# Optimization experiments

Measured on AMD Instinct MI355X. Metric: run time of the kernel, lower is better.

The kernel has to match this reference:

```python
import jax, jax.numpy as jnp
import numpy as np

N = 50000
E = 800000
D_IN, D_HID, D_OUT = 256, 512, 256
LN_EPS = 1e-5


def setup_inputs() -> dict:
    key = jax.random.key(0)
    ks = jax.random.split(key, 8)
    return {
        "v": jax.random.normal(ks[0], (N, D_IN), dtype=jnp.float32),
        "edge_weight": jax.random.uniform(ks[1], (E,), dtype=jnp.float32),
        "epsilon": jnp.zeros((1, 1), dtype=jnp.float32),
        "w1": jax.random.normal(ks[2], (D_HID, D_IN), dtype=jnp.float32) * (1.0 / np.sqrt(D_IN)),
        "b1": jnp.zeros((D_HID,), dtype=jnp.float32),
        "g1": jnp.ones((D_HID,), dtype=jnp.float32),
        "beta1": jnp.zeros((D_HID,), dtype=jnp.float32),
        "w2": jax.random.normal(ks[3], (D_OUT, D_HID), dtype=jnp.float32) * (1.0 / np.sqrt(D_HID)),
        "b2": jnp.zeros((D_OUT,), dtype=jnp.float32),
        "g2": jnp.ones((D_OUT,), dtype=jnp.float32),
        "beta2": jnp.zeros((D_OUT,), dtype=jnp.float32),
        "src": jax.random.randint(ks[4], (E,), 0, N, dtype=jnp.int32),
        "dst": jax.random.randint(ks[5], (E,), 0, N, dtype=jnp.int32),
    }


def _layer_norm(x, g, b):
    mu = jnp.mean(x, axis=-1, keepdims=True)
    var = jnp.mean(jnp.square(x - mu), axis=-1, keepdims=True)
    return (x - mu) * jax.lax.rsqrt(var + LN_EPS) * g + b


def reference(v, edge_weight, epsilon, w1, b1, g1, beta1, w2, b2, g2, beta2, src, dst):
    # sparse adjacency aggregation: agg[dst] += w * v[src]   (torch.sparse.mm(a, v))
    msgs = v[src] * edge_weight[:, None]            # [E, D_IN]
    agg = jax.ops.segment_sum(msgs, dst, num_segments=v.shape[0])  # [N, D_IN]
    h = agg + epsilon * v                            # epsilon residual
    # MLP: Linear -> LayerNorm -> ReLU  (x2)
    h = jax.nn.relu(_layer_norm(h @ w1.T + b1, g1, beta1))
    h = jax.nn.relu(_layer_norm(h @ w2.T + b2, g2, beta2))
    return h
```

## Files before the change

### kernel.cpp

```cpp
#include <hip/hip_runtime.h>

#define D_IN 256
#define D_HID 512
#define D_OUT 256
#define LN_EPS 1e-5f
#define SCAN_B 512

typedef __attribute__((ext_vector_type(8))) short bf16x8;
typedef __attribute__((ext_vector_type(4))) float f32x4;

__device__ __forceinline__ ushort f2bf(float x) {
    union { float f; unsigned u; } c; c.f = x;
    unsigned r = c.u + 0x7FFFu + ((c.u >> 16) & 1u);
    return (ushort)(r >> 16);
}
__device__ __forceinline__ float bf2f(unsigned b) {
    union { unsigned u; float f; } c; c.u = b << 16;
    return c.f;
}

__global__ void zero_kernel(int* __restrict__ p, int n) {
    int i = blockIdx.x * 256 + threadIdx.x;
    if (i < n) p[i] = 0;
}

__global__ void hist_kernel(const int* __restrict__ dst, int* __restrict__ cnt, int E) {
    int e = blockIdx.x * 256 + threadIdx.x;
    if (e < E) atomicAdd(&cnt[dst[e]], 1);
}

__global__ __launch_bounds__(SCAN_B) void scan1_kernel(const int* __restrict__ cnt,
                                                       int* __restrict__ offs,
                                                       int* __restrict__ bsum, int n) {
    __shared__ int s[SCAN_B];
    int i = blockIdx.x * SCAN_B + threadIdx.x;
    int x = (i < n) ? cnt[i] : 0;
    s[threadIdx.x] = x;
    __syncthreads();
    for (int o = 1; o < SCAN_B; o <<= 1) {
        int t = (threadIdx.x >= (unsigned)o) ? s[threadIdx.x - o] : 0;
        __syncthreads();
        s[threadIdx.x] += t;
        __syncthreads();
    }
    if (i < n) offs[i] = s[threadIdx.x] - x;
    if (threadIdx.x == SCAN_B - 1) bsum[blockIdx.x] = s[threadIdx.x];
}

__global__ __launch_bounds__(128) void scan2_kernel(int* __restrict__ bsum, int nb) {
    __shared__ int s[128];
    int x = (threadIdx.x < (unsigned)nb) ? bsum[threadIdx.x] : 0;
    s[threadIdx.x] = x;
    __syncthreads();
    for (int o = 1; o < 128; o <<= 1) {
        int t = (threadIdx.x >= (unsigned)o) ? s[threadIdx.x - o] : 0;
        __syncthreads();
        s[threadIdx.x] += t;
        __syncthreads();
    }
    if (threadIdx.x < (unsigned)nb) bsum[threadIdx.x] = s[threadIdx.x] - x;
}

__global__ __launch_bounds__(SCAN_B) void scan3_kernel(int* __restrict__ offs,
                                                       int* __restrict__ cursor,
                                                       const int* __restrict__ bsum,
                                                       int n, int E) {
    int i = blockIdx.x * SCAN_B + threadIdx.x;
    if (i < n) {
        int v0 = offs[i] + bsum[blockIdx.x];
        offs[i] = v0;
        cursor[i] = v0;
    }
    if (i == 0) offs[n] = E;
}

__global__ void fill_kernel(const int* __restrict__ src, const int* __restrict__ dst,
                            const float* __restrict__ ew, int* __restrict__ cursor,
                            int2* __restrict__ perm, int E) {
    int e = blockIdx.x * 256 + threadIdx.x;
    if (e >= E) return;
    int p = atomicAdd(&cursor[dst[e]], 1);
    perm[p] = make_int2(src[e], __float_as_int(ew[e]));
}

__global__ void cvt_bf16_kernel(const float* __restrict__ in, ushort* __restrict__ out, int n4) {
    int i = blockIdx.x * 256 + threadIdx.x;
    if (i >= n4) return;
    float4 x = ((const float4*)in)[i];
    ((ushort4*)out)[i] = make_ushort4(f2bf(x.x), f2bf(x.y), f2bf(x.z), f2bf(x.w));
}

__global__ void cvt_w_kernel(const float* __restrict__ w1, const float* __restrict__ w2,
                             ushort* __restrict__ w1b, ushort* __restrict__ w2b) {
    int i = blockIdx.x * 256 + threadIdx.x;
    const float* src; ushort* dst; int j;
    if (i < 32768) { src = w1; dst = w1b; j = i; }
    else           { src = w2; dst = w2b; j = i - 32768; }
    float4 x = ((const float4*)src)[j];
    ((ushort4*)dst)[j] = make_ushort4(f2bf(x.x), f2bf(x.y), f2bf(x.z), f2bf(x.w));
}

__global__ __launch_bounds__(256) void aggregate_kernel(
    const ushort* __restrict__ vb, const float* __restrict__ eps_p,
    const int* __restrict__ offs, const int2* __restrict__ perm,
    ushort* __restrict__ aggb, int N) {
    int node = blockIdx.x * 4 + (threadIdx.x >> 6);
    if (node >= N) return;
    int lane = threadIdx.x & 63;
    int beg = offs[node], end = offs[node + 1];
    float a0 = 0.f, a1 = 0.f, a2 = 0.f, a3 = 0.f;

    int i = beg;
    for (; i + 4 <= end; i += 4) {
        int2 p0 = perm[i + 0], p1 = perm[i + 1], p2 = perm[i + 2], p3 = perm[i + 3];
        float w0 = __int_as_float(p0.y), w1 = __int_as_float(p1.y);
        float w2 = __int_as_float(p2.y), w3 = __int_as_float(p3.y);
        ushort4 r0 = ((const ushort4*)(vb + (size_t)p0.x * D_IN))[lane];
        ushort4 r1 = ((const ushort4*)(vb + (size_t)p1.x * D_IN))[lane];
        ushort4 r2 = ((const ushort4*)(vb + (size_t)p2.x * D_IN))[lane];
        ushort4 r3 = ((const ushort4*)(vb + (size_t)p3.x * D_IN))[lane];
        a0 += w0 * bf2f(r0.x) + w1 * bf2f(r1.x) + w2 * bf2f(r2.x) + w3 * bf2f(r3.x);
        a1 += w0 * bf2f(r0.y) + w1 * bf2f(r1.y) + w2 * bf2f(r2.y) + w3 * bf2f(r3.y);
        a2 += w0 * bf2f(r0.z) + w1 * bf2f(r1.z) + w2 * bf2f(r2.z) + w3 * bf2f(r3.z);
        a3 += w0 * bf2f(r0.w) + w1 * bf2f(r1.w) + w2 * bf2f(r2.w) + w3 * bf2f(r3.w);
    }
    for (; i < end; ++i) {
        int2 p = perm[i];
        float w = __int_as_float(p.y);
        ushort4 r = ((const ushort4*)(vb + (size_t)p.x * D_IN))[lane];
        a0 += w * bf2f(r.x); a1 += w * bf2f(r.y);
        a2 += w * bf2f(r.z); a3 += w * bf2f(r.w);
    }
    float eps = eps_p[0];
    ushort4 m = ((const ushort4*)(vb + (size_t)node * D_IN))[lane];
    a0 += eps * bf2f(m.x); a1 += eps * bf2f(m.y);
    a2 += eps * bf2f(m.z); a3 += eps * bf2f(m.w);
    ((ushort4*)(aggb + (size_t)node * D_IN))[lane] =
        make_ushort4(f2bf(a0), f2bf(a1), f2bf(a2), f2bf(a3));
}

template <int COLS, int WRITE_BF16>
__global__ __launch_bounds__(256) void gemm_ln_kernel(
    const ushort* __restrict__ A, const ushort* __restrict__ B,
    const float* __restrict__ bias, const float* __restrict__ g,
    const float* __restrict__ beta, void* __restrict__ Cv, int M, int K) {
    constexpr int CW = COLS / 4;
    constexpr int CF = CW / 16;
    __shared__ ushort As[32 * 32];
    __shared__ ushort Bs[COLS * 32];
    __shared__ float red[2][32][4];
    __shared__ float mu_s[32], rs_s[32];

    int t = threadIdx.x;
    int w = t >> 6, lane = t & 63;
    int row0 = blockIdx.x * 32;
    int fr = lane & 15, q = lane >> 4, kb = q * 8;
    int lrow = lane >> 2;
    int lcol = (lane & 3) * 8;

    f32x4 acc[2][CF];
    #pragma unroll
    for (int i = 0; i < 2; ++i)
        #pragma unroll
        for (int c = 0; c < CF; ++c) {
            f32x4 z = {0.f, 0.f, 0.f, 0.f};
            acc[i][c] = z;
        }

    for (int k0 = 0; k0 < K; k0 += 32) {
        #pragma unroll
        for (int c = 0; c < CF; ++c) {
            int br = w * CW + c * 16 + lrow;
            const ushort* gp = B + (size_t)br * K + k0 + lcol;
            __builtin_amdgcn_global_load_lds(
                (const __attribute__((address_space(1))) void*)gp,
                (__attribute__((address_space(3))) void*)(&Bs[(w * CW + c * 16) * 32]),
                16, 0, 0);
        }
        if (w < 2) {
            int ar = row0 + w * 16 + lrow;
            if (ar > M - 1) ar = M - 1;
            const ushort* gp = A + (size_t)ar * K + k0 + lcol;
            __builtin_amdgcn_global_load_lds(
                (const __attribute__((address_space(1))) void*)gp,
                (__attribute__((address_space(3))) void*)(&As[(w * 16) * 32]),
                16, 0, 0);
        }
        __syncthreads();

        bf16x8 af[2], bf[CF];
        af[0] = *(const bf16x8*)&As[fr * 32 + kb];
        af[1] = *(const bf16x8*)&As[(16 + fr) * 32 + kb];
        #pragma unroll
        for (int c = 0; c < CF; ++c)
            bf[c] = *(const bf16x8*)&Bs[(w * CW + c * 16 + fr) * 32 + kb];
        #pragma unroll
        for (int i = 0; i < 2; ++i)
            #pragma unroll
            for (int c = 0; c < CF; ++c)
                acc[i][c] = __builtin_amdgcn_mfma_f32_16x16x32_bf16(af[i], bf[c], acc[i][c], 0, 0, 0);
        __syncthreads();
    }

    float bi[CF], gg[CF], bb[CF];
    #pragma unroll
    for (int c = 0; c < CF; ++c) {
        int col = w * CW + c * 16 + fr;
        bi[c] = bias[col]; gg[c] = g[col]; bb[c] = beta[col];
    }

    #pragma unroll
    for (int i = 0; i < 2; ++i) {
        #pragma unroll
        for (int r = 0; r < 4; ++r) {
            float s = 0.f, sq = 0.f;
            #pragma unroll
            for (int c = 0; c < CF; ++c) {
                float x = acc[i][c][r] + bi[c];
                acc[i][c][r] = x;
                s += x; sq += x * x;
            }
            #pragma unroll
            for (int o = 1; o < 16; o <<= 1) {
                s  += __shfl_xor(s, o, 64);
                sq += __shfl_xor(sq, o, 64);
            }
            if (fr == 0) {
                int row = i * 16 + q * 4 + r;
                red[0][row][w] = s;
                red[1][row][w] = sq;
            }
        }
    }
    __syncthreads();
    if (t < 32) {
        float s  = red[0][t][0] + red[0][t][1] + red[0][t][2] + red[0][t][3];
        float sq = red[1][t][0] + red[1][t][1] + red[1][t][2] + red[1][t][3];
        float mu = s / (float)COLS;
        float var = sq / (float)COLS - mu * mu;
        mu_s[t] = mu;
        rs_s[t] = rsqrtf(var + LN_EPS);
    }
    __syncthreads();

    #pragma unroll
    for (int i = 0; i < 2; ++i) {
        #pragma unroll
        for (int r = 0; r < 4; ++r) {
            int row = i * 16 + q * 4 + r;
            int grow = row0 + row;
            if (grow >= M) continue;
            float mu = mu_s[row], rs = rs_s[row];
            #pragma unroll
            for (int c = 0; c < CF; ++c) {
                int col = w * CW + c * 16 + fr;
                float y = (acc[i][c][r] - mu) * rs * gg[c] + bb[c];
                y = fmaxf(y, 0.f);
                if (WRITE_BF16)
                    ((ushort*)Cv)[(size_t)grow * COLS + col] = f2bf(y);
                else
                    ((float*)Cv)[(size_t)grow * COLS + col] = y;
            }
        }
    }
}

extern "C" void kernel_launch(void* const* d_in, const int* in_sizes, int n_in,
                              void* d_out, int out_size, void* d_ws, size_t ws_size,
                              hipStream_t stream) {
    const float* v     = (const float*)d_in[0];
    const float* ew    = (const float*)d_in[1];
    const float* eps   = (const float*)d_in[2];
    const float* w1    = (const float*)d_in[3];
    const float* b1    = (const float*)d_in[4];
    const float* g1    = (const float*)d_in[5];
    const float* beta1 = (const float*)d_in[6];
    const float* w2    = (const float*)d_in[7];
    const float* b2    = (const float*)d_in[8];
    const float* g2    = (const float*)d_in[9];
    const float* beta2 = (const float*)d_in[10];
    const int*   src   = (const int*)d_in[11];
    const int*   dst   = (const int*)d_in[12];

    int N = in_sizes[0] / D_IN;
    int E = in_sizes[1];

    float* out = (float*)d_out;

    char* ws = (char*)d_ws;
    size_t off = 0;
    ushort* vb   = (ushort*)(ws + off); off += (size_t)N * D_IN * 2;
    ushort* aggb = (ushort*)(ws + off); off += (size_t)N * D_IN * 2;
    ushort* h1b  = (ushort*)(ws + off); off += (size_t)N * D_HID * 2;
    ushort* w1b  = (ushort*)(ws + off); off += (size_t)D_HID * D_IN * 2;
    ushort* w2b  = (ushort*)(ws + off); off += (size_t)D_OUT * D_HID * 2;
    int* offs     = (int*)(ws + off); off += (size_t)(N + 256) * 4;
    int* cursor   = (int*)(ws + off); off += (size_t)(N + 256) * 4;
    int* bsum     = (int*)(ws + off); off += 1024;
    int2* perm    = (int2*)(ws + off); off += (size_t)E * 8;

    int nb = (N + SCAN_B - 1) / SCAN_B;

    zero_kernel<<<(N + 255) / 256, 256, 0, stream>>>(cursor, N);
    hist_kernel<<<(E + 255) / 256, 256, 0, stream>>>(dst, cursor, E);
    scan1_kernel<<<nb, SCAN_B, 0, stream>>>(cursor, offs, bsum, N);
    scan2_kernel<<<1, 128, 0, stream>>>(bsum, nb);
    scan3_kernel<<<nb, SCAN_B, 0, stream>>>(offs, cursor, bsum, N, E);
    fill_kernel<<<(E + 255) / 256, 256, 0, stream>>>(src, dst, ew, cursor, perm, E);

    cvt_bf16_kernel<<<((size_t)N * D_IN / 4 + 255) / 256, 256, 0, stream>>>(v, vb, N * D_IN / 4);
    cvt_w_kernel<<<256, 256, 0, stream>>>(w1, w2, w1b, w2b);

    aggregate_kernel<<<(N + 3) / 4, 256, 0, stream>>>(vb, eps, offs, perm, aggb, N);

    int mblocks = (N + 31) / 32;
    gemm_ln_kernel<D_HID, 1><<<mblocks, 256, 0, stream>>>(
        aggb, w1b, b1, g1, beta1, h1b, N, D_IN);

    gemm_ln_kernel<D_OUT, 0><<<mblocks, 256, 0, stream>>>(
        h1b, w2b, b2, g2, beta2, out, N, D_HID);
}
```

Baseline: 363.7 us.

## Fuse prep kernels, fold block-sum scan into scan3, enlarge GEMM tile to 64 rows

Merges the zeroing, input conversion and weight conversion launches into one prep kernel. Removes the separate single-block scan2 by having each scan3 block reduce the preceding block sums itself. Doubles the GEMM+LayerNorm row tile to 64 rows with 512 threads (8 waves), so each B-tile load from LDS is reused across more rows. The larger tile raises accumulator register pressure and cuts the block count, which may lower occupancy.

```diff
diff --git a/kernel.cpp b/kernel.cpp
--- a/kernel.cpp
+++ b/kernel.cpp
@@ -19,9 +19,32 @@
     return c.f;
 }
 
-__global__ void zero_kernel(int* __restrict__ p, int n) {
-    int i = blockIdx.x * 256 + threadIdx.x;
-    if (i < n) p[i] = 0;
+__global__ void prep_kernel(const float* __restrict__ v, const float* __restrict__ w1,
+                            const float* __restrict__ w2, ushort* __restrict__ vb,
+                            ushort* __restrict__ w1b, ushort* __restrict__ w2b,
+                            int* __restrict__ cnt, int n4v, int nzero,
+                            int bv, int bw) {
+    int b = blockIdx.x, t = threadIdx.x;
+    if (b < bv) {
+        int i = b * 256 + t;
+        if (i < n4v) {
+            float4 x = ((const float4*)v)[i];
+            ((ushort4*)vb)[i] = make_ushort4(f2bf(x.x), f2bf(x.y), f2bf(x.z), f2bf(x.w));
+        }
+    } else if (b < bv + bw) {
+        int j = (b - bv) * 256 + t;
+        if (j < 32768) {
+            float4 x = ((const float4*)w1)[j];
+            ((ushort4*)w1b)[j] = make_ushort4(f2bf(x.x), f2bf(x.y), f2bf(x.z), f2bf(x.w));
+        } else {
+            int k = j - 32768;
+            float4 x = ((const float4*)w2)[k];
+            ((ushort4*)w2b)[k] = make_ushort4(f2bf(x.x), f2bf(x.y), f2bf(x.z), f2bf(x.w));
+        }
+    } else {
+        int i = (b - bv - bw) * 256 + t;
+        if (i < nzero) cnt[i] = 0;
+    }
 }
 
 __global__ void hist_kernel(const int* __restrict__ dst, int* __restrict__ cnt, int E) {
@@ -47,27 +70,22 @@
     if (threadIdx.x == SCAN_B - 1) bsum[blockIdx.x] = s[threadIdx.x];
 }
 
-__global__ __launch_bounds__(128) void scan2_kernel(int* __restrict__ bsum, int nb) {
-    __shared__ int s[128];
-    int x = (threadIdx.x < (unsigned)nb) ? bsum[threadIdx.x] : 0;
-    s[threadIdx.x] = x;
-    __syncthreads();
-    for (int o = 1; o < 128; o <<= 1) {
-        int t = (threadIdx.x >= (unsigned)o) ? s[threadIdx.x - o] : 0;
-        __syncthreads();
-        s[threadIdx.x] += t;
-        __syncthreads();
-    }
-    if (threadIdx.x < (unsigned)nb) bsum[threadIdx.x] = s[threadIdx.x] - x;
-}
-
 __global__ __launch_bounds__(SCAN_B) void scan3_kernel(int* __restrict__ offs,
                                                        int* __restrict__ cursor,
                                                        const int* __restrict__ bsum,
-                                                       int n, int E) {
-    int i = blockIdx.x * SCAN_B + threadIdx.x;
+                                                       int n, int E, int nb) {
+    __shared__ int s[SCAN_B];
+    int t = threadIdx.x;
+    s[t] = (t < nb && t < (int)blockIdx.x) ? bsum[t] : 0;
+    __syncthreads();
+    for (int o = SCAN_B / 2; o > 0; o >>= 1) {
+        if (t < o) s[t] += s[t + o];
+        __syncthreads();
+    }
+    int base = s[0];
+    int i = blockIdx.x * SCAN_B + t;
     if (i < n) {
-        int v0 = offs[i] + bsum[blockIdx.x];
+        int v0 = offs[i] + base;
         offs[i] = v0;
         cursor[i] = v0;
     }
@@ -81,23 +99,6 @@
     if (e >= E) return;
     int p = atomicAdd(&cursor[dst[e]], 1);
     perm[p] = make_int2(src[e], __float_as_int(ew[e]));
-}
-
-__global__ void cvt_bf16_kernel(const float* __restrict__ in, ushort* __restrict__ out, int n4) {
-    int i = blockIdx.x * 256 + threadIdx.x;
-    if (i >= n4) return;
-    float4 x = ((const float4*)in)[i];
-    ((ushort4*)out)[i] = make_ushort4(f2bf(x.x), f2bf(x.y), f2bf(x.z), f2bf(x.w));
-}
-
-__global__ void cvt_w_kernel(const float* __restrict__ w1, const float* __restrict__ w2,
-                             ushort* __restrict__ w1b, ushort* __restrict__ w2b) {
-    int i = blockIdx.x * 256 + threadIdx.x;
-    const float* src; ushort* dst; int j;
-    if (i < 32768) { src = w1; dst = w1b; j = i; }
-    else           { src = w2; dst = w2b; j = i - 32768; }
-    float4 x = ((const float4*)src)[j];
-    ((ushort4*)dst)[j] = make_ushort4(f2bf(x.x), f2bf(x.y), f2bf(x.z), f2bf(x.w));
 }
 
 __global__ __launch_bounds__(256) void aggregate_kernel(
@@ -140,27 +141,27 @@
 }
 
 template <int COLS, int WRITE_BF16>
-__global__ __launch_bounds__(256) void gemm_ln_kernel(
+__global__ __launch_bounds__(512) void gemm_ln_kernel(
     const ushort* __restrict__ A, const ushort* __restrict__ B,
     const float* __restrict__ bias, const float* __restrict__ g,
     const float* __restrict__ beta, void* __restrict__ Cv, int M, int K) {
-    constexpr int CW = COLS / 4;
+    constexpr int CW = COLS / 8;
     constexpr int CF = CW / 16;
-    __shared__ ushort As[32 * 32];
+    __shared__ ushort As[64 * 32];
     __shared__ ushort Bs[COLS * 32];
-    __shared__ float red[2][32][4];
-    __shared__ float mu_s[32], rs_s[32];
+    __shared__ float red[2][64][8];
+    __shared__ float mu_s[64], rs_s[64];
 
     int t = threadIdx.x;
     int w = t >> 6, lane = t & 63;
-    int row0 = blockIdx.x * 32;
+    int row0 = blockIdx.x * 64;
     int fr = lane & 15, q = lane >> 4, kb = q * 8;
     int lrow = lane >> 2;
     int lcol = (lane & 3) * 8;
 
-    f32x4 acc[2][CF];
+    f32x4 acc[4][CF];
     #pragma unroll
-    for (int i = 0; i < 2; ++i)
+    for (int i = 0; i < 4; ++i)
         #pragma unroll
         for (int c = 0; c < CF; ++c) {
             f32x4 z = {0.f, 0.f, 0.f, 0.f};
@@ -177,7 +178,7 @@
                 (__attribute__((address_space(3))) void*)(&Bs[(w * CW + c * 16) * 32]),
                 16, 0, 0);
         }
-        if (w < 2) {
+        if (w < 4) {
             int ar = row0 + w * 16 + lrow;
             if (ar > M - 1) ar = M - 1;
             const ushort* gp = A + (size_t)ar * K + k0 + lcol;
@@ -188,14 +189,15 @@
         }
         __syncthreads();
 
-        bf16x8 af[2], bf[CF];
-        af[0] = *(const bf16x8*)&As[fr * 32 + kb];
-        af[1] = *(const bf16x8*)&As[(16 + fr) * 32 + kb];
+        bf16x8 af[4], bf[CF];
+        #pragma unroll
+        for (int i = 0; i < 4; ++i)
+            af[i] = *(const bf16x8*)&As[(i * 16 + fr) * 32 + kb];
         #pragma unroll
         for (int c = 0; c < CF; ++c)
             bf[c] = *(const bf16x8*)&Bs[(w * CW + c * 16 + fr) * 32 + kb];
         #pragma unroll
-        for (int i = 0; i < 2; ++i)
+        for (int i = 0; i < 4; ++i)
             #pragma unroll
             for (int c = 0; c < CF; ++c)
                 acc[i][c] = __builtin_amdgcn_mfma_f32_16x16x32_bf16(af[i], bf[c], acc[i][c], 0, 0, 0);
@@ -210,7 +212,7 @@
     }
 
     #pragma unroll
-    for (int i = 0; i < 2; ++i) {
+    for (int i = 0; i < 4; ++i) {
         #pragma unroll
         for (int r = 0; r < 4; ++r) {
             float s = 0.f, sq = 0.f;
@@ -233,9 +235,10 @@
         }
     }
     __syncthreads();
-    if (t < 32) {
-        float s  = red[0][t][0] + red[0][t][1] + red[0][t][2] + red[0][t][3];
-        float sq = red[1][t][0] + red[1][t][1] + red[1][t][2] + red[1][t][3];
+    if (t < 64) {
+        float s = 0.f, sq = 0.f;
+        #pragma unroll
+        for (int j = 0; j < 8; ++j) { s += red[0][t][j]; sq += red[1][t][j]; }
         float mu = s / (float)COLS;
         float var = sq / (float)COLS - mu * mu;
         mu_s[t] = mu;
@@ -244,7 +247,7 @@
     __syncthreads();
 
     #pragma unroll
-    for (int i = 0; i < 2; ++i) {
+    for (int i = 0; i < 4; ++i) {
         #pragma unroll
         for (int r = 0; r < 4; ++r) {
             int row = i * 16 + q * 4 + r;
@@ -300,23 +303,25 @@
     int2* perm    = (int2*)(ws + off); off += (size_t)E * 8;
 
     int nb = (N + SCAN_B - 1) / SCAN_B;
-
-    zero_kernel<<<(N + 255) / 256, 256, 0, stream>>>(cursor, N);
+    int n4v = N * (D_IN / 4);
+    int bv = (n4v + 255) / 256;
+    int bw = 256;
+    int bz = (N + 255) / 256;
+
+    prep_kernel<<<bv + bw + bz, 256, 0, stream>>>(v, w1, w2, vb, w1b, w2b,
+                                                  cursor, n4v, N, bv, bw);
+
     hist_kernel<<<(E + 255) / 256, 256, 0, stream>>>(dst, cursor, E);
     scan1_kernel<<<nb, SCAN_B, 0, stream>>>(cursor, offs, bsum, N);
-    scan2_kernel<<<1, 128, 0, stream>>>(bsum, nb);
-    scan3_kernel<<<nb, SCAN_B, 0, stream>>>(offs, cursor, bsum, N, E);
+    scan3_kernel<<<nb, SCAN_B, 0, stream>>>(offs, cursor, bsum, N, E, nb);
     fill_kernel<<<(E + 255) / 256, 256, 0, stream>>>(src, dst, ew, cursor, perm, E);
 
-    cvt_bf16_kernel<<<((size_t)N * D_IN / 4 + 255) / 256, 256, 0, stream>>>(v, vb, N * D_IN / 4);
-    cvt_w_kernel<<<256, 256, 0, stream>>>(w1, w2, w1b, w2b);
-
     aggregate_kernel<<<(N + 3) / 4, 256, 0, stream>>>(vb, eps, offs, perm, aggb, N);
 
-    int mblocks = (N + 31) / 32;
-    gemm_ln_kernel<D_HID, 1><<<mblocks, 256, 0, stream>>>(
+    int mblocks = (N + 63) / 64;
+    gemm_ln_kernel<D_HID, 1><<<mblocks, 512, 0, stream>>>(
         aggb, w1b, b1, g1, beta1, h1b, N, D_IN);
 
-    gemm_ln_kernel<D_OUT, 0><<<mblocks, 256, 0, stream>>>(
+    gemm_ln_kernel<D_OUT, 0><<<mblocks, 512, 0, stream>>>(
         h1b, w2b, b2, g2, beta2, out, N, D_HID);
 }
```

After: 353.8 us. 2.7% less time.
